# Kernel optimization log

Measured on AMD Instinct MI355X. Metric: run time of the kernel, lower is better.

Reference implementation:

```python
import jax, jax.numpy as jnp
import numpy as np

N, IN_DIM, OUT_DIM = 8192, 512, 512
ALPHA = 0.2  # leaky relu negative slope
NEG_BIG = -9e15

def _xavier(key, shape, gain=1.414):
    fan_in, fan_out = shape[0], shape[1]
    bound = gain * np.sqrt(6.0 / (fan_in + fan_out))
    return jax.random.uniform(key, shape, jnp.float32, -bound, bound)

def setup_inputs() -> dict:
    key = jax.random.key(0)
    k1, k2, k3, k4 = jax.random.split(key, 4)
    h = jax.random.normal(k1, (N, IN_DIM), jnp.float32)
    adj = jax.random.randint(k2, (N, N), 0, 2, jnp.int32)
    W = _xavier(k3, (IN_DIM, OUT_DIM))
    a = _xavier(k4, (2 * OUT_DIM, 1))
    return {"h": h, "adj": adj, "W": W, "a": a}

def reference(h, adj, W, a):
    Wh = h @ W                              # [N, out]
    # e_ij = leakyrelu(a1 . Wh_i + a2 . Wh_j) without the O(N^2*2d) concat
    a1 = a[:OUT_DIM, 0]                     # [out]
    a2 = a[OUT_DIM:, 0]                     # [out]
    f1 = Wh @ a1                            # [N]
    f2 = Wh @ a2                            # [N]
    e = jax.nn.leaky_relu(f1[:, None] + f2[None, :], negative_slope=ALPHA)
    e = jnp.where(adj > 0, e, NEG_BIG)
    attention = jax.nn.softmax(e, axis=1)   # dropout is identity in eval mode
    h_prime = attention @ Wh                # [N, out]
    return jax.nn.elu(h_prime)              # concat=True branch
```

## Files before the change

kernel.cpp:

```cpp
#include <hip/hip_runtime.h>
#include <stdint.h>

#define NN   8192
#define DIN  512
#define DOUT 512
#define ALPHA 0.2f

typedef float          floatx4  __attribute__((ext_vector_type(4)));
typedef float          floatx2  __attribute__((ext_vector_type(2)));
typedef short          shortx8  __attribute__((ext_vector_type(8)));
typedef unsigned short ushortx4 __attribute__((ext_vector_type(4)));
typedef int            intx2    __attribute__((ext_vector_type(2)));
typedef int            intx4    __attribute__((ext_vector_type(4)));
typedef unsigned       uintx2   __attribute__((ext_vector_type(2)));

__device__ inline unsigned short f2bf(float x) {
    union { float f; unsigned u; } v; v.f = x;
    return (unsigned short)((v.u + 0x7FFFu + ((v.u >> 16) & 1u)) >> 16);
}
__device__ inline unsigned encf(float x) {
    union { float f; unsigned u; } v; v.f = x;
    return (v.u & 0x80000000u) ? ~v.u : (v.u | 0x80000000u);
}
__device__ inline float decf(unsigned e) {
    union { float f; unsigned u; } v;
    v.u = (e & 0x80000000u) ? (e & 0x7FFFFFFFu) : ~e;
    return v.f;
}
__device__ inline float lrelu(float x) { return fmaxf(x, ALPHA * x); }

__global__ __launch_bounds__(256) void transpose_w(const float* __restrict__ W,
                                                   unsigned short* __restrict__ WT) {
    __shared__ float tile[32][33];
    const int t = threadIdx.x;
    const int x = t & 31, y = t >> 5;
    const int tr = (blockIdx.x >> 4) * 32, tc = (blockIdx.x & 15) * 32;
#pragma unroll
    for (int i = 0; i < 4; i++) {
        int r = y + i * 8;
        tile[r][x] = W[(size_t)(tr + r) * DOUT + tc + x];
    }
    __syncthreads();
#pragma unroll
    for (int i = 0; i < 4; i++) {
        int r = y + i * 8;
        WT[(size_t)(tc + r) * DIN + tr + x] = f2bf(tile[x][r]);
    }
}

__global__ __launch_bounds__(256) void gemm_wh(
    const float* __restrict__ h, const unsigned short* __restrict__ WT,
    const float* __restrict__ a, unsigned short* __restrict__ WhTt,
    float* __restrict__ f1, float* __restrict__ f2, unsigned* __restrict__ Menc)
{
    __shared__ float f1s[4][16], f2s[4][16];
    const int t = threadIdx.x;
    const int w = t >> 6, lane = t & 63, l15 = lane & 15, q = lane >> 4;
    const int r0 = blockIdx.x * 16;
    const int wc0 = w * 128;

    floatx4 acc[8];
    const floatx4 z4 = {0.f, 0.f, 0.f, 0.f};
#pragma unroll
    for (int j = 0; j < 8; j++) acc[j] = z4;

    const float* hp = &h[(size_t)(r0 + l15) * DIN + q * 8];
    const unsigned short* bp = &WT[(size_t)(wc0 + l15) * DIN + q * 8];

    floatx4 hA[2][2];
    shortx8 bB[2][8];
    hA[0][0] = *(const floatx4*)hp;
    hA[0][1] = *(const floatx4*)(hp + 4);
#pragma unroll
    for (int nt = 0; nt < 8; nt++)
        bB[0][nt] = *(const shortx8*)(bp + (size_t)nt * 16 * DIN);

#pragma unroll 2
    for (int it = 0; it < 16; ++it) {
        const int c = it & 1, n = c ^ 1;
        const int kn = ((it + 1) & 15) * 32;
        hA[n][0] = *(const floatx4*)(hp + kn);
        hA[n][1] = *(const floatx4*)(hp + kn + 4);
#pragma unroll
        for (int nt = 0; nt < 8; nt++)
            bB[n][nt] = *(const shortx8*)(bp + (size_t)nt * 16 * DIN + kn);

        shortx8 af;
#pragma unroll
        for (int j = 0; j < 8; j++)
            af[j] = (short)f2bf(hA[c][j >> 2][j & 3]);
#pragma unroll
        for (int nt = 0; nt < 8; nt++)
            acc[nt] = __builtin_amdgcn_mfma_f32_16x16x32_bf16(af, bB[c][nt], acc[nt], 0, 0, 0);
    }

    float a1v[8], a2v[8];
#pragma unroll
    for (int nt = 0; nt < 8; nt++) {
        int col = wc0 + nt * 16 + l15;
        a1v[nt] = a[col];
        a2v[nt] = a[DOUT + col];
    }
    {
        const int kk0 = r0 + q * 4;
        const int tile_k = kk0 >> 5;
        const int qq = (kk0 >> 3) & 3;
        const int j0 = kk0 & 7;
#pragma unroll
        for (int nt = 0; nt < 8; nt++) {
            const int tile_n = w * 8 + nt;
            ushortx4 pk;
#pragma unroll
            for (int reg = 0; reg < 4; reg++) pk[reg] = f2bf(acc[nt][reg]);
            *(ushortx4*)&WhTt[(((size_t)tile_k * 32 + tile_n) << 9) + qq * 128 + l15 * 8 + j0] = pk;
        }
    }
    float s1a[4], s2a[4];
#pragma unroll
    for (int reg = 0; reg < 4; reg++) {
        float s1 = 0.f, s2 = 0.f;
#pragma unroll
        for (int nt = 0; nt < 8; nt++) {
            s1 += acc[nt][reg] * a1v[nt];
            s2 += acc[nt][reg] * a2v[nt];
        }
        s1 += __shfl_xor(s1, 1, 64); s2 += __shfl_xor(s2, 1, 64);
        s1 += __shfl_xor(s1, 2, 64); s2 += __shfl_xor(s2, 2, 64);
        s1 += __shfl_xor(s1, 4, 64); s2 += __shfl_xor(s2, 4, 64);
        s1 += __shfl_xor(s1, 8, 64); s2 += __shfl_xor(s2, 8, 64);
        s1a[reg] = s1; s2a[reg] = s2;
    }
    if (l15 == 0) {
#pragma unroll
        for (int reg = 0; reg < 4; reg++) {
            f1s[w][q * 4 + reg] = s1a[reg];
            f2s[w][q * 4 + reg] = s2a[reg];
        }
    }
    __syncthreads();
    if (t < 16) {
        float v1 = f1s[0][t] + f1s[1][t] + f1s[2][t] + f1s[3][t];
        float v2 = f2s[0][t] + f2s[1][t] + f2s[2][t] + f2s[3][t];
        f1[r0 + t] = v1;
        f2[r0 + t] = v2;
        float mx = v2;
        mx = fmaxf(mx, __shfl_xor(mx, 1, 64));
        mx = fmaxf(mx, __shfl_xor(mx, 2, 64));
        mx = fmaxf(mx, __shfl_xor(mx, 4, 64));
        mx = fmaxf(mx, __shfl_xor(mx, 8, 64));
        if (t == 0) atomicMax(Menc, encf(mx));
    }
}

__global__ __launch_bounds__(1024, 4) void gat_agg(
    const int* __restrict__ adj, const unsigned short* __restrict__ WhTt,
    const float* __restrict__ f1, const float* __restrict__ f2,
    const unsigned* __restrict__ Menc, float* __restrict__ out)
{
    __shared__ __align__(16) unsigned short pbuf[2][2][64 * 40];
    __shared__ float red2[64][260];
    __shared__ float lsp[2][8][64];
    __shared__ float linv[64];

    const int t = threadIdx.x;
    const int w = t >> 6, lane = t & 63, l15 = lane & 15, q = lane >> 4;
    const int ks = w >> 3, cw = w & 7;
    const int u = (w & 7) * 64 + lane;
    const int prow = u >> 3, pk = u & 7;

    const int xcd = blockIdx.x & 7, sidx = blockIdx.x >> 3;
    const int chalf = sidx & 1;
    const int rgid = xcd * 16 + (sidx >> 1);
    const int r0 = rgid * 64;
    const int cb = chalf * 256;

    const float M = decf(*Menc);
    const float f1v = f1[r0 + prow];
    const float mi = lrelu(f1v + M);

    floatx4 acc[4][2];
    const floatx4 z4 = {0.f, 0.f, 0.f, 0.f};
#pragma unroll
    for (int i = 0; i < 4; i++)
#pragma unroll
        for (int j = 0; j < 2; j++) acc[i][j] = z4;
    float ls = 0.f;

    const unsigned short* bpp = WhTt
        + (((size_t)(ks * 128) * 32 + chalf * 16 + cw * 2) << 9) + lane * 8;
    const int* arp = adj + (size_t)(r0 + prow) * NN + ks * 4096 + pk * 4;
    const float* fpp = f2 + ks * 4096 + pk * 4;

    intx4   adjr[2];
    floatx4 ffr[2];
    shortx8 breg[2][2];

    adjr[0] = __builtin_nontemporal_load((const intx4*)arp);
    adjr[1] = __builtin_nontemporal_load((const intx4*)(arp + 32));
    ffr[0] = *(const floatx4*)fpp;
    ffr[1] = *(const floatx4*)(fpp + 32);
    {
        float p0 = __expf(lrelu(f1v + ffr[0][0]) - mi);
        float p1 = __expf(lrelu(f1v + ffr[0][1]) - mi);
        float p2 = __expf(lrelu(f1v + ffr[0][2]) - mi);
        float p3 = __expf(lrelu(f1v + ffr[0][3]) - mi);
        p0 = (adjr[0][0] > 0) ? p0 : 0.f;
        p1 = (adjr[0][1] > 0) ? p1 : 0.f;
        p2 = (adjr[0][2] > 0) ? p2 : 0.f;
        p3 = (adjr[0][3] > 0) ? p3 : 0.f;
        ls += (p0 + p1) + (p2 + p3);
        uintx2 dd;
        dd[0] = __builtin_amdgcn_perm(__float_as_uint(p1), __float_as_uint(p0), 0x07060302u);
        dd[1] = __builtin_amdgcn_perm(__float_as_uint(p3), __float_as_uint(p2), 0x07060302u);
        *(uintx2*)&pbuf[ks][0][prow * 40 + pk * 4] = dd;
    }
    breg[0][0] = *(const shortx8*)bpp;
    breg[0][1] = *(const shortx8*)(bpp + 512);
    __syncthreads();

#pragma unroll 2
    for (int it = 0; it < 128; ++it) {
        const int c = it & 1, n = c ^ 1;
        const int nx = (it + 1) & 127;
        const int nx2 = (it + 2) & 127;

        breg[n][0] = *(const shortx8*)(bpp + (size_t)nx * 16384);
        breg[n][1] = *(const shortx8*)(bpp + (size_t)nx * 16384 + 512);
        const intx4   ad_n = adjr[n];
        const floatx4 ff_n = ffr[n];
        adjr[c] = __builtin_nontemporal_load((const intx4*)(arp + nx2 * 32));
        ffr[c] = *(const floatx4*)(fpp + nx2 * 32);

        if (it < 127) {
            float p0 = __expf(lrelu(f1v + ff_n[0]) - mi);
            float p1 = __expf(lrelu(f1v + ff_n[1]) - mi);
            float p2 = __expf(lrelu(f1v + ff_n[2]) - mi);
            float p3 = __expf(lrelu(f1v + ff_n[3]) - mi);
            p0 = (ad_n[0] > 0) ? p0 : 0.f;
            p1 = (ad_n[1] > 0) ? p1 : 0.f;
            p2 = (ad_n[2] > 0) ? p2 : 0.f;
            p3 = (ad_n[3] > 0) ? p3 : 0.f;
            ls += (p0 + p1) + (p2 + p3);
            uintx2 dd;
            dd[0] = __builtin_amdgcn_perm(__float_as_uint(p1), __float_as_uint(p0), 0x07060302u);
            dd[1] = __builtin_amdgcn_perm(__float_as_uint(p3), __float_as_uint(p2), 0x07060302u);
            *(uintx2*)&pbuf[ks][n][prow * 40 + pk * 4] = dd;
        }

        const shortx8 af0 = *(const shortx8*)&pbuf[ks][c][(l15) * 40 + q * 8];
        const shortx8 af1 = *(const shortx8*)&pbuf[ks][c][(16 + l15) * 40 + q * 8];
        const shortx8 af2 = *(const shortx8*)&pbuf[ks][c][(32 + l15) * 40 + q * 8];
        const shortx8 af3 = *(const shortx8*)&pbuf[ks][c][(48 + l15) * 40 + q * 8];
#pragma unroll
        for (int nt = 0; nt < 2; nt++) {
            acc[0][nt] = __builtin_amdgcn_mfma_f32_16x16x32_bf16(af0, breg[c][nt], acc[0][nt], 0, 0, 0);
            acc[1][nt] = __builtin_amdgcn_mfma_f32_16x16x32_bf16(af1, breg[c][nt], acc[1][nt], 0, 0, 0);
            acc[2][nt] = __builtin_amdgcn_mfma_f32_16x16x32_bf16(af2, breg[c][nt], acc[2][nt], 0, 0, 0);
            acc[3][nt] = __builtin_amdgcn_mfma_f32_16x16x32_bf16(af3, breg[c][nt], acc[3][nt], 0, 0, 0);
        }
        __syncthreads();
    }

    lsp[ks][pk][prow] = ls;
    __syncthreads();
    if (t < 64) {
        float sden = 0.f;
#pragma unroll
        for (int g = 0; g < 2; g++)
#pragma unroll
            for (int kc = 0; kc < 8; kc++) sden += lsp[g][kc][t];
        linv[t] = 1.f / sden;
    }
    if (ks == 1) {
#pragma unroll
        for (int mt = 0; mt < 4; mt++)
#pragma unroll
            for (int nt = 0; nt < 2; nt++) {
                const int col = cw * 32 + nt * 16 + l15;
#pragma unroll
                for (int reg = 0; reg < 4; reg++)
                    red2[mt * 16 + q * 4 + reg][col] = acc[mt][nt][reg];
            }
    }
    __syncthreads();
    if (ks == 0) {
#pragma unroll
        for (int mt = 0; mt < 4; mt++)
#pragma unroll
            for (int nt = 0; nt < 2; nt++) {
                const int col = cw * 32 + nt * 16 + l15;
#pragma unroll
                for (int reg = 0; reg < 4; reg++) {
                    const int row = mt * 16 + q * 4 + reg;
                    float v = (acc[mt][nt][reg] + red2[row][col]) * linv[row];
                    v = (v > 0.f) ? v : (__expf(v) - 1.f);
                    out[(size_t)(r0 + row) * DOUT + cb + col] = v;
                }
            }
    }
}

extern "C" void kernel_launch(void* const* d_in, const int* in_sizes, int n_in,
                              void* d_out, int out_size, void* d_ws, size_t ws_size,
                              hipStream_t stream) {
    const float* h   = (const float*)d_in[0];
    const int*   adj = (const int*)d_in[1];
    const float* W   = (const float*)d_in[2];
    const float* a   = (const float*)d_in[3];
    float* out = (float*)d_out;

    char* ws = (char*)d_ws;
    unsigned short* WT    = (unsigned short*)ws;
    unsigned short* WhTt  = (unsigned short*)(ws + 524288);
    float*          f1    = (float*)(ws + 8912896);
    float*          f2    = (float*)(ws + 8945664);
    unsigned*       Menc  = (unsigned*)(ws + 8978432);

    hipMemsetAsync(Menc, 0, 4, stream);
    transpose_w<<<256, 256, 0, stream>>>(W, WT);
    gemm_wh<<<512, 256, 0, stream>>>(h, WT, a, WhTt, f1, f2, Menc);
    gat_agg<<<256, 1024, 0, stream>>>(adj, WhTt, f1, f2, Menc, out);
}
```

Baseline: 466.4 us.

## Split attention aggregation into 4-way K-split with partial sums and finalize kernel

The aggregation kernel now gives each block 128 rows and a quarter of the neighbour dimension, with all 512 output columns, instead of 64 rows and half the columns with an in-block 2-way K split. Each adj element is now read once instead of twice, since blocks no longer split columns. f2 is staged in shared memory. Partial numerators (4×N×512 floats) and denominators go to workspace and are reduced by a new gat_fin kernel that applies normalization and ELU. This trades about 64MB of extra partial-sum write and read traffic, plus a launch, for halving adj traffic and doubling accumulator reuse per loaded B fragment.

```diff
diff --git a/kernel.cpp b/kernel.cpp
--- a/kernel.cpp
+++ b/kernel.cpp
@@ -155,50 +155,50 @@
 __global__ __launch_bounds__(1024, 4) void gat_agg(
     const int* __restrict__ adj, const unsigned short* __restrict__ WhTt,
     const float* __restrict__ f1, const float* __restrict__ f2,
-    const unsigned* __restrict__ Menc, float* __restrict__ out)
+    const unsigned* __restrict__ Menc, float* __restrict__ P,
+    float* __restrict__ D)
 {
-    __shared__ __align__(16) unsigned short pbuf[2][2][64 * 40];
-    __shared__ float red2[64][260];
-    __shared__ float lsp[2][8][64];
-    __shared__ float linv[64];
+    __shared__ __align__(16) unsigned short pbuf[2][128 * 40];
+    __shared__ float f2s[2048];
+    __shared__ float lsp[8][128];
 
     const int t = threadIdx.x;
     const int w = t >> 6, lane = t & 63, l15 = lane & 15, q = lane >> 4;
-    const int ks = w >> 3, cw = w & 7;
-    const int u = (w & 7) * 64 + lane;
-    const int prow = u >> 3, pk = u & 7;
-
-    const int xcd = blockIdx.x & 7, sidx = blockIdx.x >> 3;
-    const int chalf = sidx & 1;
-    const int rgid = xcd * 16 + (sidx >> 1);
-    const int r0 = rgid * 64;
-    const int cb = chalf * 256;
+    const int prow = t >> 3, pk = t & 7;
+
+    const int kq = blockIdx.x & 3;
+    const int rgid = blockIdx.x >> 2;
+    const int r0 = rgid * 128;
+    const int k0 = kq * 2048;
+
+    *(floatx2*)&f2s[t * 2] = *(const floatx2*)&f2[k0 + t * 2];
 
     const float M = decf(*Menc);
     const float f1v = f1[r0 + prow];
     const float mi = lrelu(f1v + M);
 
-    floatx4 acc[4][2];
+    floatx4 acc[8][2];
     const floatx4 z4 = {0.f, 0.f, 0.f, 0.f};
 #pragma unroll
-    for (int i = 0; i < 4; i++)
+    for (int i = 0; i < 8; i++)
 #pragma unroll
         for (int j = 0; j < 2; j++) acc[i][j] = z4;
     float ls = 0.f;
 
     const unsigned short* bpp = WhTt
-        + (((size_t)(ks * 128) * 32 + chalf * 16 + cw * 2) << 9) + lane * 8;
-    const int* arp = adj + (size_t)(r0 + prow) * NN + ks * 4096 + pk * 4;
-    const float* fpp = f2 + ks * 4096 + pk * 4;
+        + (((size_t)(kq * 64) * 32 + w * 2) << 9) + lane * 8;
+    const int* arp = adj + (size_t)(r0 + prow) * NN + k0 + pk * 4;
 
     intx4   adjr[2];
     floatx4 ffr[2];
     shortx8 breg[2][2];
 
+    __syncthreads();
+
     adjr[0] = __builtin_nontemporal_load((const intx4*)arp);
     adjr[1] = __builtin_nontemporal_load((const intx4*)(arp + 32));
-    ffr[0] = *(const floatx4*)fpp;
-    ffr[1] = *(const floatx4*)(fpp + 32);
+    ffr[0] = *(const floatx4*)&f2s[pk * 4];
+    ffr[1] = *(const floatx4*)&f2s[32 + pk * 4];
     {
         float p0 = __expf(lrelu(f1v + ffr[0][0]) - mi);
         float p1 = __expf(lrelu(f1v + ffr[0][1]) - mi);
@@ -212,26 +212,26 @@
         uintx2 dd;
         dd[0] = __builtin_amdgcn_perm(__float_as_uint(p1), __float_as_uint(p0), 0x07060302u);
         dd[1] = __builtin_amdgcn_perm(__float_as_uint(p3), __float_as_uint(p2), 0x07060302u);
-        *(uintx2*)&pbuf[ks][0][prow * 40 + pk * 4] = dd;
+        *(uintx2*)&pbuf[0][prow * 40 + pk * 4] = dd;
     }
     breg[0][0] = *(const shortx8*)bpp;
     breg[0][1] = *(const shortx8*)(bpp + 512);
     __syncthreads();
 
 #pragma unroll 2
-    for (int it = 0; it < 128; ++it) {
+    for (int it = 0; it < 64; ++it) {
         const int c = it & 1, n = c ^ 1;
-        const int nx = (it + 1) & 127;
-        const int nx2 = (it + 2) & 127;
+        const int nx = (it + 1) & 63;
+        const int nx2 = (it + 2) & 63;
 
         breg[n][0] = *(const shortx8*)(bpp + (size_t)nx * 16384);
         breg[n][1] = *(const shortx8*)(bpp + (size_t)nx * 16384 + 512);
         const intx4   ad_n = adjr[n];
         const floatx4 ff_n = ffr[n];
         adjr[c] = __builtin_nontemporal_load((const intx4*)(arp + nx2 * 32));
-        ffr[c] = *(const floatx4*)(fpp + nx2 * 32);
-
-        if (it < 127) {
+        ffr[c] = *(const floatx4*)&f2s[nx2 * 32 + pk * 4];
+
+        if (it < 63) {
             float p0 = __expf(lrelu(f1v + ff_n[0]) - mi);
             float p1 = __expf(lrelu(f1v + ff_n[1]) - mi);
             float p2 = __expf(lrelu(f1v + ff_n[2]) - mi);
@@ -244,59 +244,68 @@
             uintx2 dd;
             dd[0] = __builtin_amdgcn_perm(__float_as_uint(p1), __float_as_uint(p0), 0x07060302u);
             dd[1] = __builtin_amdgcn_perm(__float_as_uint(p3), __float_as_uint(p2), 0x07060302u);
-            *(uintx2*)&pbuf[ks][n][prow * 40 + pk * 4] = dd;
-        }
-
-        const shortx8 af0 = *(const shortx8*)&pbuf[ks][c][(l15) * 40 + q * 8];
-        const shortx8 af1 = *(const shortx8*)&pbuf[ks][c][(16 + l15) * 40 + q * 8];
-        const shortx8 af2 = *(const shortx8*)&pbuf[ks][c][(32 + l15) * 40 + q * 8];
-        const shortx8 af3 = *(const shortx8*)&pbuf[ks][c][(48 + l15) * 40 + q * 8];
+            *(uintx2*)&pbuf[n][prow * 40 + pk * 4] = dd;
+        }
+
+#pragma unroll
+        for (int rg = 0; rg < 8; rg++) {
+            const shortx8 af = *(const shortx8*)&pbuf[c][(rg * 16 + l15) * 40 + q * 8];
+            acc[rg][0] = __builtin_amdgcn_mfma_f32_16x16x32_bf16(af, breg[c][0], acc[rg][0], 0, 0, 0);
+            acc[rg][1] = __builtin_amdgcn_mfma_f32_16x16x32_bf16(af, breg[c][1], acc[rg][1], 0, 0, 0);
+        }
+        __syncthreads();
+    }
+
+    lsp[pk][prow] = ls;
+    __syncthreads();
+    if (t < 128) {
+        float s = 0.f;
+#pragma unroll
+        for (int kc = 0; kc < 8; kc++) s += lsp[kc][t];
+        D[kq * NN + r0 + t] = s;
+    }
+
+    float* Pq = P + (size_t)kq * ((size_t)NN * DOUT) + (size_t)r0 * DOUT;
+#pragma unroll
+    for (int rg = 0; rg < 8; rg++)
 #pragma unroll
         for (int nt = 0; nt < 2; nt++) {
-            acc[0][nt] = __builtin_amdgcn_mfma_f32_16x16x32_bf16(af0, breg[c][nt], acc[0][nt], 0, 0, 0);
-            acc[1][nt] = __builtin_amdgcn_mfma_f32_16x16x32_bf16(af1, breg[c][nt], acc[1][nt], 0, 0, 0);
-            acc[2][nt] = __builtin_amdgcn_mfma_f32_16x16x32_bf16(af2, breg[c][nt], acc[2][nt], 0, 0, 0);
-            acc[3][nt] = __builtin_amdgcn_mfma_f32_16x16x32_bf16(af3, breg[c][nt], acc[3][nt], 0, 0, 0);
-        }
-        __syncthreads();
-    }
-
-    lsp[ks][pk][prow] = ls;
-    __syncthreads();
-    if (t < 64) {
-        float sden = 0.f;
-#pragma unroll
-        for (int g = 0; g < 2; g++)
-#pragma unroll
-            for (int kc = 0; kc < 8; kc++) sden += lsp[g][kc][t];
-        linv[t] = 1.f / sden;
-    }
-    if (ks == 1) {
-#pragma unroll
-        for (int mt = 0; mt < 4; mt++)
-#pragma unroll
-            for (int nt = 0; nt < 2; nt++) {
-                const int col = cw * 32 + nt * 16 + l15;
-#pragma unroll
-                for (int reg = 0; reg < 4; reg++)
-                    red2[mt * 16 + q * 4 + reg][col] = acc[mt][nt][reg];
+            const int col = w * 32 + nt * 16 + l15;
+#pragma unroll
+            for (int reg = 0; reg < 4; reg++) {
+                const int row = rg * 16 + q * 4 + reg;
+                __builtin_nontemporal_store(acc[rg][nt][reg],
+                                            Pq + (size_t)row * DOUT + col);
             }
-    }
-    __syncthreads();
-    if (ks == 0) {
-#pragma unroll
-        for (int mt = 0; mt < 4; mt++)
-#pragma unroll
-            for (int nt = 0; nt < 2; nt++) {
-                const int col = cw * 32 + nt * 16 + l15;
-#pragma unroll
-                for (int reg = 0; reg < 4; reg++) {
-                    const int row = mt * 16 + q * 4 + reg;
-                    float v = (acc[mt][nt][reg] + red2[row][col]) * linv[row];
-                    v = (v > 0.f) ? v : (__expf(v) - 1.f);
-                    out[(size_t)(r0 + row) * DOUT + cb + col] = v;
-                }
-            }
+        }
+}
+
+__global__ __launch_bounds__(1024) void gat_fin(
+    const float* __restrict__ P, const float* __restrict__ D,
+    float* __restrict__ out)
+{
+    const int t = threadIdx.x;
+    const int r0 = blockIdx.x * 32;
+    const int rr = t >> 7;
+    const int c4 = (t & 127) * 4;
+    const size_t Q = (size_t)NN * DOUT;
+#pragma unroll
+    for (int j = 0; j < 4; j++) {
+        const int row = r0 + j * 8 + rr;
+        const float den = ((D[row] + D[NN + row]) + (D[2 * NN + row] + D[3 * NN + row]));
+        const float li = 1.f / den;
+        const size_t off = (size_t)row * DOUT + c4;
+        floatx4 v0 = __builtin_nontemporal_load((const floatx4*)(P + off));
+        floatx4 v1 = __builtin_nontemporal_load((const floatx4*)(P + Q + off));
+        floatx4 v2 = __builtin_nontemporal_load((const floatx4*)(P + 2 * Q + off));
+        floatx4 v3 = __builtin_nontemporal_load((const floatx4*)(P + 3 * Q + off));
+        floatx4 s;
+#pragma unroll
+        for (int i = 0; i < 4; i++) {
+            float x = ((v0[i] + v1[i]) + (v2[i] + v3[i])) * li;
+            s[i] = (x > 0.f) ? x : (__expf(x) - 1.f);
+        }
+        __builtin_nontemporal_store(s, (floatx4*)(out + off));
     }
 }
 
@@ -315,9 +324,12 @@
     float*          f1    = (float*)(ws + 8912896);
     float*          f2    = (float*)(ws + 8945664);
     unsigned*       Menc  = (unsigned*)(ws + 8978432);
+    float*          D     = (float*)(ws + 9437184);
+    float*          P     = (float*)(ws + 16777216);
 
     hipMemsetAsync(Menc, 0, 4, stream);
     transpose_w<<<256, 256, 0, stream>>>(W, WT);
     gemm_wh<<<512, 256, 0, stream>>>(h, WT, a, WhTt, f1, f2, Menc);
-    gat_agg<<<256, 1024, 0, stream>>>(adj, WhTt, f1, f2, Menc, out);
-}
+    gat_agg<<<256, 1024, 0, stream>>>(adj, WhTt, f1, f2, Menc, P, D);
+    gat_fin<<<256, 1024, 0, stream>>>(P, D, out);
+}
```

After: 470.5 us. About the same (+0.9%).
